# Kernel tuning notes

Measured on AMD Instinct MI355X. Metric: run time of the kernel, lower is better.

Reference implementation:

```python
import jax, jax.numpy as jnp
import numpy as np

CROP_H, CROP_W = 14, 14
MAX_BS = 64  # max boxes per image per level (MoldBatch padding)
NUM_LEVELS = 4


def _crop_and_resize(fmap, boxes, box_indices, ch, cw):
    """Bilinear tf.image.crop_and_resize equivalent.
    fmap: [B,H,W,C]; boxes: [N,4] normalized (y1,x1,y2,x2); box_indices: [N] int32.
    Returns [N,ch,cw,C]; samples outside the image get extrapolation value 0."""
    B, H, W, C = fmap.shape
    y1, x1, y2, x2 = boxes[:, 0], boxes[:, 1], boxes[:, 2], boxes[:, 3]
    ty = jnp.arange(ch, dtype=boxes.dtype) / (ch - 1)
    tx = jnp.arange(cw, dtype=boxes.dtype) / (cw - 1)
    ys = y1[:, None] * (H - 1) + ty[None, :] * ((y2 - y1)[:, None] * (H - 1))  # [N,ch]
    xs = x1[:, None] * (W - 1) + tx[None, :] * ((x2 - x1)[:, None] * (W - 1))  # [N,cw]
    y0f = jnp.floor(ys); x0f = jnp.floor(xs)
    wy = (ys - y0f)[:, :, None, None]  # [N,ch,1,1]
    wx = (xs - x0f)[:, None, :, None]  # [N,1,cw,1]
    y0 = jnp.clip(y0f.astype(jnp.int32), 0, H - 1); y1i = jnp.clip(y0 + 1, 0, H - 1)
    x0 = jnp.clip(x0f.astype(jnp.int32), 0, W - 1); x1i = jnp.clip(x0 + 1, 0, W - 1)
    bi = box_indices[:, None, None]
    g = lambda yi, xi: fmap[bi, yi[:, :, None], xi[:, None, :], :]  # [N,ch,cw,C]
    top = g(y0, x0) * (1 - wx) + g(y0, x1i) * wx
    bot = g(y1i, x0) * (1 - wx) + g(y1i, x1i) * wx
    out = top * (1 - wy) + bot * wy
    valid = ((ys >= 0) & (ys <= H - 1))[:, :, None] & ((xs >= 0) & (xs <= W - 1))[:, None, :]
    return out * valid[..., None].astype(out.dtype)


def setup_inputs() -> dict:
    key = jax.random.key(0)
    ks = jax.random.split(key, 8)
    B, N, C = 4, 128, 256
    sizes = [256, 128, 64, 32]
    inp = {}
    for i, s in enumerate(sizes):
        inp[f"fmap{i}"] = jax.random.normal(ks[i], (B, s, s, C), dtype=jnp.float32)
    ids = jax.random.randint(ks[4], (B, N), 0, NUM_LEVELS).astype(jnp.float32)
    cxy = jax.random.uniform(ks[5], (B, N, 2), minval=0.0, maxval=1024.0)
    wh = jax.random.uniform(ks[6], (B, N, 2), minval=16.0, maxval=256.0)
    cls_id = jnp.zeros((B, N, 1), jnp.float32)
    conf = jnp.full((B, N, 1), 0.9, jnp.float32)
    inp["dist_boxes"] = jnp.concatenate([ids[..., None], cxy, wh, cls_id, conf], axis=-1)
    inp["images"] = jnp.zeros((B, 1024, 1024, 3), jnp.float32)
    return inp


def _forward(fmaps, dist_boxes, images):
    B, N, _ = dist_boxes.shape
    Hi, Wi = images.shape[1], images.shape[2]
    cx, cy, w, h = (dist_boxes[..., 1], dist_boxes[..., 2], dist_boxes[..., 3], dist_boxes[..., 4])
    # NormalizeBoxes: (cx,cy,w,h) pixels -> normalized (y1,x1,y2,x2) for crop_and_resize
    norm_boxes = jnp.stack([
        (cy - h / 2) / (Hi - 1), (cx - w / 2) / (Wi - 1),
        (cy + h / 2) / (Hi - 1), (cx + w / 2) / (Wi - 1)], axis=-1)  # [B,N,4]
    ids = dist_boxes[..., 0]
    flat_boxes = norm_boxes.reshape(B * N, 4)
    box_idx = jnp.repeat(jnp.arange(B, dtype=jnp.int32), N)
    b_idx = jnp.broadcast_to(jnp.arange(B)[:, None], (B, N))
    boxes6 = dist_boxes[..., 1:]  # [B,N,6]
    roi_fmaps, roi_boxes = [], []
    for lvl, fmap in enumerate(fmaps):
        C = fmap.shape[-1]
        mask = ids == lvl  # [B,N] level routing (tf.where/gather_nd equivalent)
        crops = _crop_and_resize(fmap, flat_boxes, box_idx, CROP_H, CROP_W)
        crops = crops.reshape(B, N, CROP_H, CROP_W, C)
        # MoldBatch: scatter level-l boxes densely per image, zero-padded to MAX_BS
        rank = jnp.cumsum(mask.astype(jnp.int32), axis=1) - 1
        dest = jnp.where(mask & (rank < MAX_BS), rank, MAX_BS)  # overflow -> dump slot
        pf = jnp.zeros((B, MAX_BS + 1, CROP_H, CROP_W, C), crops.dtype)
        pf = pf.at[b_idx, dest].set(crops * mask[..., None, None, None].astype(crops.dtype))
        roi_fmaps.append(pf[:, :MAX_BS])
        pb = jnp.zeros((B, MAX_BS + 1, 6), dist_boxes.dtype)
        pb = pb.at[b_idx, dest].set(boxes6 * mask[..., None].astype(boxes6.dtype))
        roi_boxes.append(pb[:, :MAX_BS])
    return jnp.stack(roi_fmaps), jnp.concatenate(roi_boxes, axis=1)


def reference(fmap0, fmap1, fmap2, fmap3, dist_boxes, images):
    return _forward([fmap0, fmap1, fmap2, fmap3], dist_boxes, images)
```

## Files before the change

### kernel.cpp

```cpp
#include <hip/hip_runtime.h>

#define CROP 14
#define MAXBS 64
#define NLVL 4
#define BDIM 4
#define NBOX 128
#define CCH 256
#define NSL (NLVL * BDIM * MAXBS)
#define NBLK (NSL * CROP)

typedef float f32x4 __attribute__((ext_vector_type(4)));

__global__ void roi_meta_kernel(const float* __restrict__ db,
                                int* __restrict__ slot_map,
                                float* __restrict__ out1) {
    int b = blockIdx.x;
    int t = threadIdx.x;
    __shared__ int lvl_arr[NBOX];
    __shared__ int smap[NLVL * MAXBS];

    if (t < NBOX) {
        lvl_arr[t] = (int)db[(b * NBOX + t) * 7 + 0];
    }
    smap[t] = -1;
    __syncthreads();

    if (t < NLVL) {
        int r = 0;
        for (int n = 0; n < NBOX; ++n) {
            if (lvl_arr[n] == t) {
                if (r < MAXBS) smap[t * MAXBS + r] = n;
                r++;
            }
        }
    }
    __syncthreads();

    int n = smap[t];
    int lvl = t >> 6;
    int slot = t & 63;
    slot_map[(lvl * BDIM + b) * MAXBS + slot] = n;

    float* o = out1 + ((size_t)(b * (NLVL * MAXBS) + t)) * 6;
    if (n >= 0) {
        const float* src = db + (b * NBOX + n) * 7 + 1;
        #pragma unroll
        for (int j = 0; j < 6; ++j) o[j] = src[j];
    } else {
        #pragma unroll
        for (int j = 0; j < 6; ++j) o[j] = 0.f;
    }
}

__global__ __launch_bounds__(256) void roi_crop_kernel(
        const float* __restrict__ f0,
        const float* __restrict__ f1,
        const float* __restrict__ f2,
        const float* __restrict__ f3,
        const float* __restrict__ db,
        const int* __restrict__ slot_map,
        float* __restrict__ out0) {
    int bid = blockIdx.x;
    int y  = bid % CROP;
    int sl = bid / CROP;
    int t  = threadIdx.x;
    int cq = t & 63;
    int xg = t >> 6;

    f32x4* out = (f32x4*)(out0 + ((size_t)(sl * CROP + y)) * CROP * CCH);

    int n = slot_map[sl];
    if (n < 0) {
        f32x4 z = {0.f, 0.f, 0.f, 0.f};
        #pragma unroll
        for (int xi = 0; xi < 4; ++xi) {
            int x = xg + xi * 4;
            if (x < CROP) __builtin_nontemporal_store(z, &out[x * 64 + cq]);
        }
        return;
    }

    int lvl = sl >> 8;
    int b   = (sl >> 6) & 3;
    int s   = 256 >> lvl;
    const float* f = (lvl == 0) ? f0 : (lvl == 1) ? f1 : (lvl == 2) ? f2 : f3;

    const float* bx = db + (b * NBOX + n) * 7;
    float cx = bx[1], cy = bx[2], w = bx[3], h = bx[4];

    float y1n = (cy - h * 0.5f) / 1023.0f;
    float x1n = (cx - w * 0.5f) / 1023.0f;
    float y2n = (cy + h * 0.5f) / 1023.0f;
    float x2n = (cx + w * 0.5f) / 1023.0f;

    float Hm1 = (float)(s - 1);
    float ty = (float)y / 13.0f;
    float ys = y1n * Hm1 + ty * ((y2n - y1n) * Hm1);
    float y0f = floorf(ys);
    float wy = ys - y0f;
    int iy0 = (int)y0f;
    iy0 = iy0 < 0 ? 0 : (iy0 > s - 1 ? s - 1 : iy0);
    int iy1 = iy0 + 1;
    if (iy1 > s - 1) iy1 = s - 1;
    bool vy = (ys >= 0.f) && (ys <= Hm1);

    const f32x4* rowT = (const f32x4*)(f + ((size_t)(b * s + iy0)) * s * CCH);
    const f32x4* rowB = (const f32x4*)(f + ((size_t)(b * s + iy1)) * s * CCH);

    float x1nH   = x1n * Hm1;
    float xscale = (x2n - x1n) * Hm1;
    float omwy = 1.f - wy;

    #pragma unroll
    for (int xi = 0; xi < 4; ++xi) {
        int x = xg + xi * 4;
        if (x >= CROP) break;

        float xs = x1nH + ((float)x / 13.0f) * xscale;
        float x0f = floorf(xs);
        float wx = xs - x0f;
        int ix0 = (int)x0f;
        ix0 = ix0 < 0 ? 0 : (ix0 > s - 1 ? s - 1 : ix0);
        int ix1 = ix0 + 1;
        if (ix1 > s - 1) ix1 = s - 1;
        bool vx = (xs >= 0.f) && (xs <= Hm1);

        f32x4 a  = rowT[ix0 * 64 + cq];
        f32x4 bv = rowT[ix1 * 64 + cq];
        f32x4 cv = rowB[ix0 * 64 + cq];
        f32x4 dv = rowB[ix1 * 64 + cq];

        float omwx = 1.f - wx;
        f32x4 top = a  * omwx + bv * wx;
        f32x4 bot = cv * omwx + dv * wx;
        f32x4 v   = top * omwy + bot * wy;

        if (!(vy && vx)) v = (f32x4){0.f, 0.f, 0.f, 0.f};
        __builtin_nontemporal_store(v, &out[x * 64 + cq]);
    }
}

extern "C" void kernel_launch(void* const* d_in, const int* in_sizes, int n_in,
                              void* d_out, int out_size, void* d_ws, size_t ws_size,
                              hipStream_t stream) {
    const float* f0 = (const float*)d_in[0];
    const float* f1 = (const float*)d_in[1];
    const float* f2 = (const float*)d_in[2];
    const float* f3 = (const float*)d_in[3];
    const float* db = (const float*)d_in[4];

    float* out0 = (float*)d_out;
    float* out1 = out0 + (size_t)NSL * CROP * CROP * CCH;
    int* slot_map = (int*)d_ws;

    roi_meta_kernel<<<BDIM, 256, 0, stream>>>(db, slot_map, out1);
    roi_crop_kernel<<<NBLK, 256, 0, stream>>>(
        f0, f1, f2, f3, db, slot_map, out0);
}
```

Baseline: 463.4 us.

## Process seven crop rows per block instead of one row per block

Each block now handles half of a ROI slot (7 output rows) instead of one row, so the grid shrinks from NSL*14 to NSL*2 blocks. The box decode and the per-column x indices and weights are computed once and reused across the rows. The aim is to cut per-block launch and setup overhead. The cost is fewer blocks in flight and serial row loops, which may hide memory latency less well in a bandwidth-bound gather/store kernel.

```diff
diff --git a/kernel.cpp b/kernel.cpp
--- a/kernel.cpp
+++ b/kernel.cpp
@@ -7,7 +7,8 @@
 #define NBOX 128
 #define CCH 256
 #define NSL (NLVL * BDIM * MAXBS)
-#define NBLK (NSL * CROP)
+#define YHALF 7
+#define NBLK (NSL * 2)
 
 typedef float f32x4 __attribute__((ext_vector_type(4)));
 
@@ -60,22 +61,26 @@
         const float* __restrict__ db,
         const int* __restrict__ slot_map,
         float* __restrict__ out0) {
-    int bid = blockIdx.x;
-    int y  = bid % CROP;
-    int sl = bid / CROP;
+    int bid  = blockIdx.x;
+    int sl   = bid >> 1;
+    int half = bid & 1;
+    int y0   = half * YHALF;
     int t  = threadIdx.x;
     int cq = t & 63;
     int xg = t >> 6;
 
-    f32x4* out = (f32x4*)(out0 + ((size_t)(sl * CROP + y)) * CROP * CCH);
+    f32x4* outsl = (f32x4*)(out0 + ((size_t)sl) * CROP * CROP * CCH);
 
     int n = slot_map[sl];
     if (n < 0) {
         f32x4 z = {0.f, 0.f, 0.f, 0.f};
-        #pragma unroll
-        for (int xi = 0; xi < 4; ++xi) {
-            int x = xg + xi * 4;
-            if (x < CROP) __builtin_nontemporal_store(z, &out[x * 64 + cq]);
+        for (int y = y0; y < y0 + YHALF; ++y) {
+            #pragma unroll
+            for (int xi = 0; xi < 4; ++xi) {
+                int x = xg + xi * 4;
+                if (x < CROP)
+                    __builtin_nontemporal_store(z, &outsl[(y * CROP + x) * 64 + cq]);
+            }
         }
         return;
     }
@@ -94,49 +99,65 @@
     float x2n = (cx + w * 0.5f) / 1023.0f;
 
     float Hm1 = (float)(s - 1);
-    float ty = (float)y / 13.0f;
-    float ys = y1n * Hm1 + ty * ((y2n - y1n) * Hm1);
-    float y0f = floorf(ys);
-    float wy = ys - y0f;
-    int iy0 = (int)y0f;
-    iy0 = iy0 < 0 ? 0 : (iy0 > s - 1 ? s - 1 : iy0);
-    int iy1 = iy0 + 1;
-    if (iy1 > s - 1) iy1 = s - 1;
-    bool vy = (ys >= 0.f) && (ys <= Hm1);
-
-    const f32x4* rowT = (const f32x4*)(f + ((size_t)(b * s + iy0)) * s * CCH);
-    const f32x4* rowB = (const f32x4*)(f + ((size_t)(b * s + iy1)) * s * CCH);
-
     float x1nH   = x1n * Hm1;
     float xscale = (x2n - x1n) * Hm1;
-    float omwy = 1.f - wy;
+    float y1nH   = y1n * Hm1;
+    float yscale = (y2n - y1n) * Hm1;
 
+    int   ix0[4], ix1[4];
+    float wx[4];
+    bool  vx[4];
     #pragma unroll
     for (int xi = 0; xi < 4; ++xi) {
         int x = xg + xi * 4;
-        if (x >= CROP) break;
-
         float xs = x1nH + ((float)x / 13.0f) * xscale;
         float x0f = floorf(xs);
-        float wx = xs - x0f;
-        int ix0 = (int)x0f;
-        ix0 = ix0 < 0 ? 0 : (ix0 > s - 1 ? s - 1 : ix0);
-        int ix1 = ix0 + 1;
-        if (ix1 > s - 1) ix1 = s - 1;
-        bool vx = (xs >= 0.f) && (xs <= Hm1);
+        wx[xi] = xs - x0f;
+        int i0 = (int)x0f;
+        i0 = i0 < 0 ? 0 : (i0 > s - 1 ? s - 1 : i0);
+        int i1 = i0 + 1;
+        if (i1 > s - 1) i1 = s - 1;
+        ix0[xi] = i0;
+        ix1[xi] = i1;
+        vx[xi] = (xs >= 0.f) && (xs <= Hm1);
+    }
 
-        f32x4 a  = rowT[ix0 * 64 + cq];
-        f32x4 bv = rowT[ix1 * 64 + cq];
-        f32x4 cv = rowB[ix0 * 64 + cq];
-        f32x4 dv = rowB[ix1 * 64 + cq];
+    const f32x4* fb = (const f32x4*)(f + ((size_t)b) * s * s * CCH);
 
-        float omwx = 1.f - wx;
-        f32x4 top = a  * omwx + bv * wx;
-        f32x4 bot = cv * omwx + dv * wx;
-        f32x4 v   = top * omwy + bot * wy;
+    for (int y = y0; y < y0 + YHALF; ++y) {
+        float ty = (float)y / 13.0f;
+        float ys = y1nH + ty * yscale;
+        float y0f = floorf(ys);
+        float wy = ys - y0f;
+        int iy0 = (int)y0f;
+        iy0 = iy0 < 0 ? 0 : (iy0 > s - 1 ? s - 1 : iy0);
+        int iy1 = iy0 + 1;
+        if (iy1 > s - 1) iy1 = s - 1;
+        bool vy = (ys >= 0.f) && (ys <= Hm1);
+        float omwy = 1.f - wy;
 
-        if (!(vy && vx)) v = (f32x4){0.f, 0.f, 0.f, 0.f};
-        __builtin_nontemporal_store(v, &out[x * 64 + cq]);
+        const f32x4* rowT = fb + (size_t)iy0 * s * 64;
+        const f32x4* rowB = fb + (size_t)iy1 * s * 64;
+        f32x4* outrow = outsl + (size_t)(y * CROP) * 64;
+
+        #pragma unroll
+        for (int xi = 0; xi < 4; ++xi) {
+            int x = xg + xi * 4;
+            if (x >= CROP) break;
+
+            f32x4 a  = rowT[ix0[xi] * 64 + cq];
+            f32x4 bv = rowT[ix1[xi] * 64 + cq];
+            f32x4 cv = rowB[ix0[xi] * 64 + cq];
+            f32x4 dv = rowB[ix1[xi] * 64 + cq];
+
+            float omwx = 1.f - wx[xi];
+            f32x4 top = a  * omwx + bv * wx[xi];
+            f32x4 bot = cv * omwx + dv * wx[xi];
+            f32x4 v   = top * omwy + bot * wy;
+
+            if (!(vy && vx[xi])) v = (f32x4){0.f, 0.f, 0.f, 0.f};
+            __builtin_nontemporal_store(v, &outrow[x * 64 + cq]);
+        }
     }
 }
 
```

Measured after the change: 480.0 us. 3.6% more time.
